# Performance work log

Hardware: AMD Instinct MI355X
Metric: run time of the kernel (lower is better)

## Reference

```python
import jax, jax.numpy as jnp
import numpy as np

H, N, RANK = 256, 64, 1
SEQ_L = 8192


def setup_inputs() -> dict:
    key = jax.random.key(0)
    ks = jax.random.split(key, 12)
    # timescales dt in [1e-3, 1e-1] -> log_dt uniform in [log 1e-3, log 1e-1]
    log_dt = jax.random.uniform(ks[0], (H,), jnp.float32,
                                minval=np.log(1e-3), maxval=np.log(1e-1))
    def cplx(kr, ki, shape, scale=1.0):
        return (scale * jax.random.normal(kr, shape, jnp.float32),
                scale * jax.random.normal(ki, shape, jnp.float32))
    C_re, C_im = cplx(ks[1], ks[2], (1, H, N))
    B_re, B_im = cplx(ks[3], ks[4], (1, H, N))
    P_re, P_im = cplx(ks[5], ks[6], (RANK, H, N), scale=0.5)
    Q_re, Q_im = cplx(ks[7], ks[8], (RANK, H, N), scale=0.5)
    # HiPPO-NPLR-like poles: Re(w) < 0 (Hurwitz), Im(w) = pi*n ladder
    w_re = -(0.5 + 0.5 * jax.random.uniform(ks[9], (H, N), jnp.float32))
    w_im = jnp.broadcast_to(np.pi * jnp.arange(N, dtype=jnp.float32), (H, N))
    return {
        "log_dt": log_dt,
        "C_re": C_re, "C_im": C_im,
        "B_re": B_re, "B_im": B_im,
        "P_re": P_re, "P_im": P_im,
        "Q_re": Q_re, "Q_im": Q_im,
        "w_re": w_re, "w_im": w_im,
        "L": SEQ_L,
    }


def reference(log_dt, C_re, C_im, B_re, B_im, P_re, P_im, Q_re, Q_im,
              w_re, w_im, L):
    # SSKernelNPLR.forward with rate=1.0, state=None, rank=1.
    Lf = L // 2 + 1
    dt = jnp.exp(log_dt)                                   # (H,)
    w = (w_re + 1j * w_im).astype(jnp.complex64)           # (H, N)
    B = (B_re + 1j * B_im).astype(jnp.complex64)           # (1, H, N)
    C = (C_re + 1j * C_im).astype(jnp.complex64)           # (1, H, N)
    P = (P_re + 1j * P_im).astype(jnp.complex64)           # (r, H, N)
    Q = (Q_re + 1j * Q_im).astype(jnp.complex64)           # (r, H, N)

    # bilinear-transform FFT nodes
    omega = jnp.exp((-2j * jnp.pi / L) * jnp.arange(Lf)).astype(jnp.complex64)  # (Lf,)
    z = 2.0 * (1.0 - omega) / (1.0 + omega)                # (Lf,)

    wdt = w * dt[:, None]                                  # (H, N)
    Bc = jnp.concatenate([B, P], axis=0)                   # (1+r, H, N)
    Cc = jnp.concatenate([C, Q], axis=0)                   # (1+r, H, N)
    v = Bc[None, :, :, :] * Cc[:, None, :, :]              # (1+r, 1+r, H, N)

    # Cauchy kernel: r[a,b,h,l] = sum_n v[a,b,h,n] / (z[l] - wdt[h,n])
    recip = 1.0 / (z[None, None, :] - wdt[:, :, None])     # (H, N, Lf)
    r = jnp.einsum('abhn,hnl->abhl', v, recip)             # (1+r, 1+r, H, Lf)
    r = r * dt[None, None, :, None]

    # rank-1 Woodbury correction
    k_f = r[:1, :1] - r[:1, 1:] * r[1:, :1] / (1.0 + r[1:, 1:])  # (1, 1, H, Lf)
    k_f = k_f * 2.0 / (1.0 + omega)

    k = jnp.fft.irfft(k_f, n=L, axis=-1)[..., :L]          # (1, 1, H, L) real
    k_B = k[-1]                                            # (1, H, L)
    return k_B
```

## Files before the change

### kernel.cpp

```cpp
#include <hip/hip_runtime.h>
#include <hip/hip_fp16.h>
#include <math.h>

#define HDIM 256
#define NDIM 64
#define LDIM 8192
#define LF   4097
#define MDIM 4096
#define LOG2M 12
#define TWN  4096

typedef _Float16 f16x8 __attribute__((ext_vector_type(8)));
typedef float    f32x4 __attribute__((ext_vector_type(4)));

__device__ __forceinline__ int cvt_pk_f16(float lo, float hi) {
    union { __half2 h; int i; } u;
    u.h = __floats2half2_rn(lo, hi);
    return u.i;
}

__device__ __forceinline__ int spad(int i) { return i + (i >> 4); }

__global__ __launch_bounds__(1024, 4) void fused_kernel(
    const float* __restrict__ log_dt,
    const float* __restrict__ C_re, const float* __restrict__ C_im,
    const float* __restrict__ B_re, const float* __restrict__ B_im,
    const float* __restrict__ P_re, const float* __restrict__ P_im,
    const float* __restrict__ Q_re, const float* __restrict__ Q_im,
    const float* __restrict__ w_re, const float* __restrict__ w_im,
    float2* __restrict__ out2)
{
    __shared__ float2 kfs[LF];
    __shared__ float2 S[MDIM + MDIM / 16];
    __shared__ float2 TW[TWN + TWN / 16];

    const int h    = blockIdx.x;
    const int tid  = threadIdx.x;
    const int lane = tid & 63;
    const int wave = tid >> 6;
    const int g    = lane >> 4;
    const int m    = lane & 15;
    const float dt = expf(log_dt[h]);
    const int hb   = h * NDIM;

    for (int p = tid; p < TWN; p += 1024) {
        float s, c;
        sincosf((3.14159265358979323846f / (float)TWN) * (float)p, &s, &c);
        TW[spad(p)] = make_float2(c, s);
    }

    if (tid < 64) {
        const float br = B_re[hb + lane], bi = B_im[hb + lane];
        const float cr = C_re[hb + lane], ci = C_im[hb + lane];
        float sr = cr * br - ci * bi;
        float si = cr * bi + ci * br;
        #pragma unroll
        for (int off = 32; off > 0; off >>= 1) {
            sr += __shfl_xor(sr, off);
            si += __shfl_xor(si, off);
        }
        if (tid == 0)
            kfs[MDIM] = make_float2(0.5f * dt * sr, 0.5f * dt * si);
    }

    float nwr_[16], nw2_[16], wi_[16];
    int   av[4][4];
    {
        const bool arow = (m < 8);
        const int  ai   = m >> 1;
        const int  c    = m & 1;
        const float* fre = (ai >= 2) ? Q_re : C_re;
        const float* fim = (ai >= 2) ? Q_im : C_im;
        const float* sre = (ai & 1) ? P_re : B_re;
        const float* sim = (ai & 1) ? P_im : B_im;
        #pragma unroll
        for (int q = 0; q < 4; ++q) {
            #pragma unroll
            for (int t = 0; t < 4; ++t) {
                const int n = hb + 16 * q + 4 * g + t;
                const float nw = -w_re[n] * dt;
                nwr_[q * 4 + t] = nw;
                nw2_[q * 4 + t] = nw * nw;
                wi_[q * 4 + t]  = w_im[n] * dt;
                float e0 = 0.f, e1 = 0.f;
                if (arow) {
                    const float fr = fre[n], fi = fim[n];
                    const float s2r = sre[n], s2i = sim[n];
                    const float vr = fr * s2r - fi * s2i;
                    const float vi = fr * s2i + fi * s2r;
                    e0 = c ? vi : vr;
                    e1 = c ? vr : -vi;
                }
                av[q][t] = cvt_pk_f16(e0, e1);
            }
        }
    }

    const int lbase = wave * 256 + m;

    float ch, sh;
    {
        const float a0 = (3.14159265358979323846f / (float)LDIM) * (float)lbase;
        sincosf(a0, &sh, &ch);
    }
    const float cd = 0.99998117528260114265f;
    const float sd = 0.00613588464915447536f;

    #pragma unroll 2
    for (int t16 = 0; t16 < 16; ++t16) {
        const float zt = 2.f * sh * __builtin_amdgcn_rcpf(ch);

        f32x4 acc0 = {0.f, 0.f, 0.f, 0.f};
        f32x4 acc1 = {0.f, 0.f, 0.f, 0.f};
        #pragma unroll
        for (int q = 0; q < 4; ++q) {
            int bv[4];
            #pragma unroll
            for (int t = 0; t < 4; ++t) {
                const float tim = zt - wi_[q * 4 + t];
                const float den = fmaf(tim, tim, nw2_[q * 4 + t]);
                const float rc  = __builtin_amdgcn_rcpf(den);
                bv[t] = cvt_pk_f16(nwr_[q * 4 + t] * rc, -(tim * rc));
            }
            union { int i[4]; f16x8 v; } ua, ub;
            ua.i[0] = av[q][0]; ua.i[1] = av[q][1];
            ua.i[2] = av[q][2]; ua.i[3] = av[q][3];
            ub.i[0] = bv[0]; ub.i[1] = bv[1]; ub.i[2] = bv[2]; ub.i[3] = bv[3];
            if (q < 2)
                acc0 = __builtin_amdgcn_mfma_f32_16x16x32_f16(ua.v, ub.v, acc0, 0, 0, 0);
            else
                acc1 = __builtin_amdgcn_mfma_f32_16x16x32_f16(ua.v, ub.v, acc1, 0, 0, 0);
        }
        const f32x4 acc = acc0 + acc1;

        const float o0 = __shfl_xor(acc[0], 16);
        const float o1 = __shfl_xor(acc[1], 16);
        const float o2 = __shfl_xor(acc[2], 16);
        const float o3 = __shfl_xor(acc[3], 16);
        if (lane < 16) {
            const int l = lbase + t16 * 16;
            const float numr = acc[2] * o0 - acc[3] * o1;
            const float numi = acc[2] * o1 + acc[3] * o0;
            const float d_r  = 1.f + dt * o2;
            const float d_i  = dt * o3;
            const float dd   = fmaf(d_r, d_r, d_i * d_i);
            const float rr2  = __builtin_amdgcn_rcpf(dd);
            const float cr = dt * ((numr * d_r + numi * d_i) * rr2);
            const float ci = dt * ((numi * d_r - numr * d_i) * rr2);
            const float Tr = acc[0] - cr;
            const float Ti = acc[1] - ci;
            const float Ei = 0.5f * dt * zt;
            kfs[l] = make_float2(dt * Tr - Ei * Ti, dt * Ti + Ei * Tr);
        }

        const float chn = ch * cd - sh * sd;
        const float shn = sh * cd + ch * sd;
        ch = chn; sh = shn;
    }

    __syncthreads();

    for (int l = tid; l <= MDIM / 2; l += 1024) {
        const float2 Kl = kfs[l];
        const float2 Km = kfs[MDIM - l];
        const float Ar = 0.5f * (Kl.x + Km.x);
        const float Ai = 0.5f * (Kl.y - Km.y);
        const float Br = 0.5f * (Kl.x - Km.x);
        const float Bi = 0.5f * (Kl.y + Km.y);
        const float2 w = TW[spad(l)];
        const float Or = w.x * Br - w.y * Bi;
        const float Oi = w.x * Bi + w.y * Br;
        const int bl = (int)(__brev((unsigned)l) >> (32 - LOG2M));
        S[spad(bl)] = make_float2(Ar - Oi, Ai + Or);
        if (l > 0 && l < MDIM / 2) {
            const int bm = (int)(__brev((unsigned)(MDIM - l)) >> (32 - LOG2M));
            S[spad(bm)] = make_float2(Ar + Oi, Or - Ai);
        }
    }

    #pragma unroll
    for (int stage = 0; stage < LOG2M; ++stage) {
        const int half = 1 << stage;
        __syncthreads();
        #pragma unroll 2
        for (int t = tid; t < MDIM / 2; t += 1024) {
            const int pos = t & (half - 1);
            const int i0  = ((t & ~(half - 1)) << 1) | pos;
            const int i1  = i0 + half;
            const float2 w = TW[spad(pos << (LOG2M - stage))];
            const float2 a = S[spad(i0)];
            const float2 b = S[spad(i1)];
            const float tr = w.x * b.x - w.y * b.y;
            const float ti = w.x * b.y + w.y * b.x;
            S[spad(i0)] = make_float2(a.x + tr, a.y + ti);
            S[spad(i1)] = make_float2(a.x - tr, a.y - ti);
        }
    }
    __syncthreads();

    const float invM = 1.f / (float)MDIM;
    for (int n = tid; n < MDIM; n += 1024) {
        const float2 z = S[spad(n)];
        out2[(size_t)h * MDIM + n] = make_float2(z.x * invM, z.y * invM);
    }
}

extern "C" void kernel_launch(void* const* d_in, const int* in_sizes, int n_in,
                              void* d_out, int out_size, void* d_ws, size_t ws_size,
                              hipStream_t stream)
{
    const float* log_dt = (const float*)d_in[0];
    const float* C_re   = (const float*)d_in[1];
    const float* C_im   = (const float*)d_in[2];
    const float* B_re   = (const float*)d_in[3];
    const float* B_im   = (const float*)d_in[4];
    const float* P_re   = (const float*)d_in[5];
    const float* P_im   = (const float*)d_in[6];
    const float* Q_re   = (const float*)d_in[7];
    const float* Q_im   = (const float*)d_in[8];
    const float* w_re   = (const float*)d_in[9];
    const float* w_im   = (const float*)d_in[10];

    float2* out2 = (float2*)d_out;

    fused_kernel<<<HDIM, 1024, 0, stream>>>(log_dt, C_re, C_im, B_re, B_im,
                                            P_re, P_im, Q_re, Q_im,
                                            w_re, w_im, out2);
}
```

Baseline: 38.92 us.

## Alias spectrum buffer into FFT scratch and halve twiddle table to cut LDS

```diff
diff --git a/kernel.cpp b/kernel.cpp
--- a/kernel.cpp
+++ b/kernel.cpp
@@ -8,7 +8,7 @@
 #define LF   4097
 #define MDIM 4096
 #define LOG2M 12
-#define TWN  4096
+#define TWN  2048
 
 typedef _Float16 f16x8 __attribute__((ext_vector_type(8)));
 typedef float    f32x4 __attribute__((ext_vector_type(4)));
@@ -21,7 +21,7 @@
 
 __device__ __forceinline__ int spad(int i) { return i + (i >> 4); }
 
-__global__ __launch_bounds__(1024, 4) void fused_kernel(
+__global__ __launch_bounds__(1024, 8) void fused_kernel(
     const float* __restrict__ log_dt,
     const float* __restrict__ C_re, const float* __restrict__ C_im,
     const float* __restrict__ B_re, const float* __restrict__ B_im,
@@ -30,8 +30,7 @@
     const float* __restrict__ w_re, const float* __restrict__ w_im,
     float2* __restrict__ out2)
 {
-    __shared__ float2 kfs[LF];
-    __shared__ float2 S[MDIM + MDIM / 16];
+    __shared__ float2 S[MDIM + MDIM / 16 + 1];
     __shared__ float2 TW[TWN + TWN / 16];
 
     const int h    = blockIdx.x;
@@ -43,10 +42,12 @@
     const float dt = expf(log_dt[h]);
     const int hb   = h * NDIM;
 
-    for (int p = tid; p < TWN; p += 1024) {
+    {
         float s, c;
-        sincosf((3.14159265358979323846f / (float)TWN) * (float)p, &s, &c);
-        TW[spad(p)] = make_float2(c, s);
+        sincosf((3.14159265358979323846f / (float)TWN) * (float)tid, &s, &c);
+        TW[spad(tid)] = make_float2(c, s);
+        sincosf((3.14159265358979323846f / (float)TWN) * (float)(tid + 1024), &s, &c);
+        TW[spad(tid + 1024)] = make_float2(c, s);
     }
 
     if (tid < 64) {
@@ -60,7 +61,7 @@
             si += __shfl_xor(si, off);
         }
         if (tid == 0)
-            kfs[MDIM] = make_float2(0.5f * dt * sr, 0.5f * dt * si);
+            S[spad(MDIM)] = make_float2(0.5f * dt * sr, 0.5f * dt * si);
     }
 
     float nwr_[16], nw2_[16], wi_[16];
@@ -150,7 +151,7 @@
             const float Tr = acc[0] - cr;
             const float Ti = acc[1] - ci;
             const float Ei = 0.5f * dt * zt;
-            kfs[l] = make_float2(dt * Tr - Ei * Ti, dt * Ti + Ei * Tr);
+            S[spad(l)] = make_float2(dt * Tr - Ei * Ti, dt * Ti + Ei * Tr);
         }
 
         const float chn = ch * cd - sh * sd;
@@ -160,22 +161,51 @@
 
     __syncthreads();
 
-    for (int l = tid; l <= MDIM / 2; l += 1024) {
-        const float2 Kl = kfs[l];
-        const float2 Km = kfs[MDIM - l];
-        const float Ar = 0.5f * (Kl.x + Km.x);
-        const float Ai = 0.5f * (Kl.y - Km.y);
-        const float Br = 0.5f * (Kl.x - Km.x);
-        const float Bi = 0.5f * (Kl.y + Km.y);
-        const float2 w = TW[spad(l)];
-        const float Or = w.x * Br - w.y * Bi;
-        const float Oi = w.x * Bi + w.y * Br;
-        const int bl = (int)(__brev((unsigned)l) >> (32 - LOG2M));
+    const int l0 = tid;
+    const int l1 = tid + 1024;
+    const float2 Kl0 = S[spad(l0)];
+    const float2 Km0 = S[spad(MDIM - l0)];
+    const float2 Kl1 = S[spad(l1)];
+    const float2 Km1 = S[spad(MDIM - l1)];
+    float2 K2;
+    if (tid == 0) K2 = S[spad(2048)];
+
+    float w0s, w0c;
+    sincosf((3.14159265358979323846f / (float)MDIM) * (float)l0, &w0s, &w0c);
+    const float r2 = 0.70710678118654752440f;
+    const float w1c = (w0c - w0s) * r2;
+    const float w1s = (w0s + w0c) * r2;
+
+    __syncthreads();
+
+    {
+        const float Ar = 0.5f * (Kl0.x + Km0.x);
+        const float Ai = 0.5f * (Kl0.y - Km0.y);
+        const float Br = 0.5f * (Kl0.x - Km0.x);
+        const float Bi = 0.5f * (Kl0.y + Km0.y);
+        const float Or = w0c * Br - w0s * Bi;
+        const float Oi = w0c * Bi + w0s * Br;
+        const int bl = (int)(__brev((unsigned)l0) >> (32 - LOG2M));
         S[spad(bl)] = make_float2(Ar - Oi, Ai + Or);
-        if (l > 0 && l < MDIM / 2) {
-            const int bm = (int)(__brev((unsigned)(MDIM - l)) >> (32 - LOG2M));
+        if (l0 > 0) {
+            const int bm = (int)(__brev((unsigned)(MDIM - l0)) >> (32 - LOG2M));
             S[spad(bm)] = make_float2(Ar + Oi, Or - Ai);
         }
+    }
+    {
+        const float Ar = 0.5f * (Kl1.x + Km1.x);
+        const float Ai = 0.5f * (Kl1.y - Km1.y);
+        const float Br = 0.5f * (Kl1.x - Km1.x);
+        const float Bi = 0.5f * (Kl1.y + Km1.y);
+        const float Or = w1c * Br - w1s * Bi;
+        const float Oi = w1c * Bi + w1s * Br;
+        const int bl = (int)(__brev((unsigned)l1) >> (32 - LOG2M));
+        S[spad(bl)] = make_float2(Ar - Oi, Ai + Or);
+        const int bm = (int)(__brev((unsigned)(MDIM - l1)) >> (32 - LOG2M));
+        S[spad(bm)] = make_float2(Ar + Oi, Or - Ai);
+    }
+    if (tid == 0) {
+        S[spad(1)] = make_float2(K2.x, -K2.y);
     }
 
     #pragma unroll
@@ -187,7 +217,7 @@
             const int pos = t & (half - 1);
             const int i0  = ((t & ~(half - 1)) << 1) | pos;
             const int i1  = i0 + half;
-            const float2 w = TW[spad(pos << (LOG2M - stage))];
+            const float2 w = TW[spad(pos << (LOG2M - 1 - stage))];
             const float2 a = S[spad(i0)];
             const float2 b = S[spad(i1)];
             const float tr = w.x * b.x - w.y * b.y;
```

Measured after the change: 55.76 us. 1.43x slower.
